# Kernel optimization log

Hardware: AMD Instinct MI355X
Metric: run time of the kernel (lower is better)

The kernel has to match this reference:

```python
import jax, jax.numpy as jnp
import numpy as np
from jax import lax


def _quadrature_weights(bw):
    # s2cnn-style Driscoll-Healy quadrature weights over beta, length 2*bw
    j = np.arange(2 * bw)
    k = np.arange(bw)
    theta = np.pi * (2 * j + 1) / (4 * bw)
    s = (np.sin(np.outer(2 * j + 1, 2 * k + 1) * np.pi / (4 * bw)) / (2 * k + 1)).sum(-1)
    return jnp.asarray((2.0 / bw) * np.sin(theta) * s, jnp.float32)


def _conv2d(x, W, b):
    y = lax.conv_general_dilated(x, W, (1, 1), 'SAME',
                                 dimension_numbers=('NCHW', 'OIHW', 'NCHW'))
    return y + b[None, :, None, None]


def setup_inputs() -> dict:
    key = jax.random.key(0)
    ks = jax.random.split(key, 8)
    b, n = 8, 32768
    res_pt, res_r = 32, 8
    inputs = jax.random.normal(ks[0], (b, n, 3), jnp.float32)
    return {
        'inputs': inputs,
        'scale': jnp.float32(3.0),      # max radius covered by radial bins
        'sigma': jnp.float32(0.5),      # gaussian width in grid units
        'A': jnp.float32(1.0),          # splat amplitude
        'inteval_comp': jnp.float32(0.5),
        'res_pt': res_pt,
        'res_r': res_r,
        'W_s2_1': 0.08 * jax.random.normal(ks[1], (32, 8, 3, 3), jnp.float32),
        'b_s2_1': jnp.zeros((32,), jnp.float32),
        'W_s2_2': 0.05 * jax.random.normal(ks[2], (64, 32, 3, 3), jnp.float32),
        'b_s2_2': jnp.zeros((64,), jnp.float32),
        'W_gamma': 0.1 * jax.random.normal(ks[3], (64, 32), jnp.float32),
        'W_c3_1': 0.05 * jax.random.normal(ks[4], (64, 128), jnp.float32),
        'b_c3_1': jnp.zeros((64,), jnp.float32),
        'W_c3_2': 0.05 * jax.random.normal(ks[5], (32, 64), jnp.float32),
        'b_c3_2': jnp.zeros((32,), jnp.float32),
    }


def reference(inputs, scale, sigma, A, inteval_comp, res_pt, res_r,
              W_s2_1, b_s2_1, W_s2_2, b_s2_2, W_gamma,
              W_c3_1, b_c3_1, W_c3_2, b_c3_2):
    b, n, _ = inputs.shape
    # ---- remap: cartesian -> spherical with min-radius clamp (utils.remap) ----
    x, y, z = inputs[..., 0], inputs[..., 1], inputs[..., 2]
    r = jnp.maximum(jnp.sqrt(x * x + y * y + z * z), 0.1)
    theta = jnp.arccos(jnp.clip(z / r, -1.0, 1.0))            # [0, pi]
    phi = jnp.arctan2(y, x) + np.pi                            # [0, 2pi)
    # ---- s2_gridding: gaussian-weighted point -> (theta,phi,r) grid scatter ----
    ct = theta / np.pi * res_pt                                # continuous bin coords
    cp = phi / (2 * np.pi) * res_pt
    cr = r / scale * res_r
    it = jnp.clip(jnp.floor(ct).astype(jnp.int32), 0, res_pt - 1)
    ip = jnp.clip(jnp.floor(cp).astype(jnp.int32), 0, res_pt - 1)
    ir = jnp.clip(jnp.floor(cr).astype(jnp.int32), 0, res_r - 1)
    d2 = ((ct - (it + inteval_comp)) ** 2
          + (cp - (ip + inteval_comp)) ** 2
          + (cr - (ir + inteval_comp)) ** 2)
    w = A * jnp.exp(-d2 / (2.0 * sigma * sigma))               # (b, n)
    vals = jnp.stack([w, w * x, w * y, w * z], axis=-1)        # (b, n, 4)
    bidx = jnp.arange(b, dtype=jnp.int32)[:, None] * jnp.ones((1, n), jnp.int32)
    flat = ((bidx * res_pt + it) * res_pt + ip) * res_r + ir   # (b, n)
    grid = jnp.zeros((b * res_pt * res_pt * res_r, 4), jnp.float32)
    grid = grid.at[flat.reshape(-1)].add(vals.reshape(-1, 4))
    grid = grid.reshape(b, res_pt, res_pt, res_r, 4)
    ft = jnp.transpose(grid[..., 0], (0, 3, 1, 2))             # (b, res_r, res_pt, res_pt)
    # ---- encoder_l1 (s2cnn_equators): S2 convs + gamma lift to SO3 grid ----
    h = jax.nn.relu(_conv2d(ft, W_s2_1, b_s2_1))
    h = jax.nn.relu(_conv2d(h, W_s2_2, b_s2_2))                # (b, 64, res_pt, res_pt)
    ft_grid = jnp.einsum('bcxy,cg->bcxyg', h, W_gamma)         # (b, 64, rp, rp, rp)
    # ---- so3_integrate: quadrature weight over beta, sum alpha/gamma ----
    wq = _quadrature_weights(res_pt // 2)                      # (res_pt,)
    ft_max = jnp.einsum('bcxyg,y->bc', ft_grid, wq)            # (b, 64)
    # ---- broadcast global feature, concat, pointwise conv3d head ----
    ft_max_ = jnp.broadcast_to(ft_max[:, :, None, None, None],
                               (b, ft_grid.shape[1], res_pt, res_pt, res_pt))
    cat = jnp.concatenate([ft_grid, ft_max_], axis=1)          # (b, 128, rp, rp, rp)
    h3 = jax.nn.relu(jnp.einsum('bcxyg,dc->bdxyg', cat, W_c3_1)
                     + b_c3_1[None, :, None, None, None])
    out = (jnp.einsum('bdxyg,ed->bexyg', h3, W_c3_2)
           + b_c3_2[None, :, None, None, None])                # (b, 32, rp, rp, rp)
    ft_g = out.reshape(b, out.shape[1], -1).max(-1)            # (b, 32)
    return (out, ft_g)
```

## Files before the change

kernel.cpp:

```cpp
#include <hip/hip_runtime.h>
#include <math.h>

#define PI_D 3.14159265358979323846
#define PI_F 3.14159265358979323846f

typedef _Float16 half8 __attribute__((ext_vector_type(8)));
typedef _Float16 half2v __attribute__((ext_vector_type(2)));
typedef float floatx4 __attribute__((ext_vector_type(4)));
#define MFMA16(a,b,c) __builtin_amdgcn_mfma_f32_16x16x32_f16(a,b,c,0,0,0)

__global__ void k_scatter(const float* __restrict__ inp,
                          const float* __restrict__ p_scale,
                          const float* __restrict__ p_sigma,
                          const float* __restrict__ p_A,
                          const float* __restrict__ p_ic,
                          float* __restrict__ ft) {
  int i = blockIdx.x * 256 + threadIdx.x;
  float scale = p_scale[0];
  float sigma = p_sigma[0];
  float A     = p_A[0];
  float icomp = p_ic[0];
  int b = i >> 15;
  float x = inp[i*3+0];
  float y = inp[i*3+1];
  float z = inp[i*3+2];
  float r = sqrtf(x*x + y*y + z*z);
  r = fmaxf(r, 0.1f);
  float ctv = fminf(fmaxf(z / r, -1.0f), 1.0f);
  float theta = acosf(ctv);
  float phi = atan2f(y, x) + PI_F;
  float ct = theta * (32.0f / PI_F);
  float cp = phi * (32.0f / (2.0f * PI_F));
  float cr = r / scale * 8.0f;
  int it = (int)floorf(ct); it = min(max(it, 0), 31);
  int ip = (int)floorf(cp); ip = min(max(ip, 0), 31);
  int ir = (int)floorf(cr); ir = min(max(ir, 0), 7);
  float dt = ct - ((float)it + icomp);
  float dp = cp - ((float)ip + icomp);
  float dr = cr - ((float)ir + icomp);
  float d2 = dt*dt + dp*dp + dr*dr;
  float w = A * expf(-d2 / (2.0f * sigma * sigma));
  atomicAdd(&ft[((b*8 + ir)*32 + it)*32 + ip], w);
}

__global__ void k_wq(float* __restrict__ wq) {
  int t = threadIdx.x;
  double jj = 2.0*(double)t + 1.0;
  double theta = PI_D * jj / 64.0;
  double s = 0.0;
  for (int k = 0; k < 16; ++k)
    s += sin(jj * (double)(2*k+1) * PI_D / 64.0) / (double)(2*k+1);
  wq[t] = (float)((2.0/16.0) * sin(theta) * s);
}

__global__ void k_prepV(const float* __restrict__ Wg, const float* __restrict__ Wc31,
                        _Float16* __restrict__ VswH, _Float16* __restrict__ VswL) {
  int flat = blockIdx.x * 256 + threadIdx.x;
  int jj = flat & 7;
  int l  = (flat >> 3) & 63;
  int rest = flat >> 9;
  int ks = rest & 1, mt = rest >> 1;
  int c = ks*32 + (l >> 4)*8 + jj;
  int m = mt*16 + (l & 15);
  int g = m >> 6, d = m & 63;
  float val = Wg[c*32 + g] * Wc31[d*128 + c];
  _Float16 hi = (_Float16)val;
  _Float16 lo = (_Float16)(val - (float)hi);
  VswH[flat] = hi;
  VswL[flat] = lo;
}

__global__ void k_prepW2(const float* __restrict__ Wc32,
                         _Float16* __restrict__ W2swH, _Float16* __restrict__ W2swL) {
  int flat = blockIdx.x * 256 + threadIdx.x;
  int jj = flat & 7;
  int l  = (flat >> 3) & 63;
  int rest = flat >> 9;
  int ks = rest & 1, mt2 = rest >> 1;
  int e = mt2*16 + (l & 15);
  int d = ks*32 + (l >> 4)*8 + jj;
  float val = Wc32[e*64 + d];
  _Float16 hi = (_Float16)val;
  _Float16 lo = (_Float16)(val - (float)hi);
  W2swH[flat] = hi;
  W2swL[flat] = lo;
}

__global__ void k_conv1(const float* __restrict__ ft, const float* __restrict__ W,
                        const float* __restrict__ bias, float* __restrict__ h1) {
  int blk = blockIdx.x;
  int b = blk >> 5, oc = blk & 31;
  __shared__ float Ws[72];
  int t = threadIdx.x;
  if (t < 72) Ws[t] = W[oc*72 + t];
  __syncthreads();
  int x = t >> 5, y = t & 31;
  float acc = bias[oc];
  const float* fb = ft + b*8192;
  for (int ic = 0; ic < 8; ++ic) {
    const float* fc = fb + ic*1024;
    const float* wr = Ws + ic*9;
#pragma unroll
    for (int dx = -1; dx <= 1; ++dx) {
      int xx = x + dx;
      bool okx = ((unsigned)xx < 32u);
#pragma unroll
      for (int dy = -1; dy <= 1; ++dy) {
        int yy = y + dy;
        float v = (okx && ((unsigned)yy < 32u)) ? fc[xx*32 + yy] : 0.f;
        acc = fmaf(v, wr[(dx+1)*3 + (dy+1)], acc);
      }
    }
  }
  h1[(b*32 + oc)*1024 + t] = fmaxf(acc, 0.f);
}

__global__ __launch_bounds__(512) void k_conv2(const float* __restrict__ h1,
                        const float* __restrict__ W,
                        const float* __restrict__ bias, float* __restrict__ h2) {
  int blk = blockIdx.x;
  int b = blk >> 5, q = blk & 31;
  int oc0 = (q >> 1) * 4, xh = q & 1;
  __shared__ float Ws[4*288];
  int t = threadIdx.x;
  for (int idx = t; idx < 4*288; idx += 512) Ws[idx] = W[oc0*288 + idx];
  __syncthreads();
  int x = xh*16 + (t >> 5), y = t & 31;
  float a0 = bias[oc0+0], a1 = bias[oc0+1], a2 = bias[oc0+2], a3 = bias[oc0+3];
  const float* hb = h1 + b*32*1024;
  for (int ic = 0; ic < 32; ++ic) {
    const float* hc = hb + ic*1024;
    const float* w0 = Ws + 0*288 + ic*9;
    const float* w1 = Ws + 1*288 + ic*9;
    const float* w2 = Ws + 2*288 + ic*9;
    const float* w3 = Ws + 3*288 + ic*9;
#pragma unroll
    for (int dx = -1; dx <= 1; ++dx) {
      int xx = x + dx;
      bool okx = ((unsigned)xx < 32u);
#pragma unroll
      for (int dy = -1; dy <= 1; ++dy) {
        int yy = y + dy;
        float v = (okx && ((unsigned)yy < 32u)) ? hc[xx*32 + yy] : 0.f;
        int k = (dx+1)*3 + (dy+1);
        a0 = fmaf(v, w0[k], a0);
        a1 = fmaf(v, w1[k], a1);
        a2 = fmaf(v, w2[k], a2);
        a3 = fmaf(v, w3[k], a3);
      }
    }
  }
  int p = x*32 + y;
  h2[(b*64 + oc0+0)*1024 + p] = fmaxf(a0, 0.f);
  h2[(b*64 + oc0+1)*1024 + p] = fmaxf(a1, 0.f);
  h2[(b*64 + oc0+2)*1024 + p] = fmaxf(a2, 0.f);
  h2[(b*64 + oc0+3)*1024 + p] = fmaxf(a3, 0.f);
}

__global__ void k_reduce(const float* __restrict__ h2, const float* __restrict__ Wg,
                         const float* __restrict__ wq, float* __restrict__ ftmax) {
  int blk = blockIdx.x;
  int b = blk >> 6, c = blk & 63;
  __shared__ float wqs[32];
  __shared__ float red[256];
  int t = threadIdx.x;
  if (t < 32) wqs[t] = wq[t];
  __syncthreads();
  const float* hb = h2 + (b*64 + c)*1024;
  float acc = 0.f;
  for (int i = t; i < 1024; i += 256) acc = fmaf(hb[i], wqs[i & 31], acc);
  red[t] = acc;
  __syncthreads();
  for (int s2 = 128; s2 > 0; s2 >>= 1) {
    if (t < s2) red[t] += red[t + s2];
    __syncthreads();
  }
  if (t == 0) {
    float sg = 0.f;
    for (int g = 0; g < 32; ++g) sg += Wg[c*32 + g];
    ftmax[b*64 + c] = sg * red[0];
  }
}

__global__ __launch_bounds__(512) void k_head(
    const float* __restrict__ h2, const float* __restrict__ ftmax,
    const float* __restrict__ Wc31, const float* __restrict__ bc31,
    const float* __restrict__ bc32,
    const half8* __restrict__ VswH, const half8* __restrict__ VswL,
    const half8* __restrict__ W2swH, const half8* __restrict__ W2swL,
    float* __restrict__ out, float* __restrict__ blockmax) {
  __shared__ __align__(16) _Float16 h3H[512*72];
  __shared__ __align__(16) _Float16 h3L[512*72];
  __shared__ __align__(16) _Float16 h2H[32*72];
  __shared__ __align__(16) _Float16 h2L[32*72];
  __shared__ float Ks[64];
  __shared__ float vbuf2[8*16];
  int blk = blockIdx.x;
  int b = blk >> 5, x = blk & 31;
  int t = threadIdx.x;
  int lane = t & 63, w = t >> 6;
  int n16 = lane & 15, quad = lane >> 4;

  for (int idx = t; idx < 2048; idx += 512) {
    int c = idx & 63, y = idx >> 6;
    float v = h2[(b*64 + c)*1024 + x*32 + y];
    _Float16 hi = (_Float16)v;
    h2H[y*72 + c] = hi;
    h2L[y*72 + c] = (_Float16)(v - (float)hi);
  }
  if (t < 64) {
    float acc = bc31[t];
    for (int c = 0; c < 64; ++c)
      acc = fmaf(Wc31[t*128 + 64 + c], ftmax[b*64 + c], acc);
    Ks[t] = acc;
  }
  __syncthreads();

  half8 bh00, bh01, bh10, bh11, bl00, bl01, bl10, bl11;
  {
    int a00 = (0*16 + n16)*72 + 0*32 + quad*8;
    int a01 = (0*16 + n16)*72 + 1*32 + quad*8;
    int a10 = (1*16 + n16)*72 + 0*32 + quad*8;
    int a11 = (1*16 + n16)*72 + 1*32 + quad*8;
    bh00 = *(const half8*)&h2H[a00];  bl00 = *(const half8*)&h2L[a00];
    bh01 = *(const half8*)&h2H[a01];  bl01 = *(const half8*)&h2L[a01];
    bh10 = *(const half8*)&h2H[a10];  bl10 = *(const half8*)&h2L[a10];
    bh11 = *(const half8*)&h2H[a11];  bl11 = *(const half8*)&h2L[a11];
  }
  int mt2 = w & 1;
  half8 a2h0 = W2swH[(mt2*2 + 0)*64 + lane];
  half8 a2h1 = W2swH[(mt2*2 + 1)*64 + lane];
  half8 a2l0 = W2swL[(mt2*2 + 0)*64 + lane];
  half8 a2l1 = W2swL[(mt2*2 + 1)*64 + lane];
  float bias_e[4];
#pragma unroll
  for (int r = 0; r < 4; ++r) bias_e[r] = bc32[mt2*16 + quad*4 + r];

  float vmax[4] = {-3.4e38f, -3.4e38f, -3.4e38f, -3.4e38f};

  for (int h = 0; h < 2; ++h) {
    if (h) __syncthreads();
    for (int i = 0; i < 8; ++i) {
      int mt = h*64 + w*8 + i;
      half8 ah0 = VswH[(mt*2 + 0)*64 + lane];
      half8 ah1 = VswH[(mt*2 + 1)*64 + lane];
      half8 al0 = VswL[(mt*2 + 0)*64 + lane];
      half8 al1 = VswL[(mt*2 + 1)*64 + lane];
      floatx4 acc0 = {0.f, 0.f, 0.f, 0.f};
      floatx4 acc1 = {0.f, 0.f, 0.f, 0.f};
      acc0 = MFMA16(ah0, bh00, acc0);  acc1 = MFMA16(ah0, bh10, acc1);
      acc0 = MFMA16(ah0, bl00, acc0);  acc1 = MFMA16(ah0, bl10, acc1);
      acc0 = MFMA16(al0, bh00, acc0);  acc1 = MFMA16(al0, bh10, acc1);
      acc0 = MFMA16(ah1, bh01, acc0);  acc1 = MFMA16(ah1, bh11, acc1);
      acc0 = MFMA16(ah1, bl01, acc0);  acc1 = MFMA16(ah1, bl11, acc1);
      acc0 = MFMA16(al1, bh01, acc0);  acc1 = MFMA16(al1, bh11, acc1);
      int g = mt >> 2, gl = g & 15;
      int dbase = (mt & 3)*16 + quad*4;
      float4 kv = *(const float4*)&Ks[dbase];
#pragma unroll
      for (int nt = 0; nt < 2; ++nt) {
        floatx4 a = nt ? acc1 : acc0;
        int y = nt*16 + n16;
        int rowc = y*16 + gl;
        int dsw = (dbase + y*8) & 63;
        float v0 = fmaxf(a[0] + kv.x, 0.f);
        float v1 = fmaxf(a[1] + kv.y, 0.f);
        float v2 = fmaxf(a[2] + kv.z, 0.f);
        float v3 = fmaxf(a[3] + kv.w, 0.f);
        _Float16 c0 = (_Float16)v0, c1 = (_Float16)v1, c2 = (_Float16)v2, c3 = (_Float16)v3;
        half2v hh0 = {c0, c1}, hh1 = {c2, c3};
        half2v ll0 = {(_Float16)(v0 - (float)c0), (_Float16)(v1 - (float)c1)};
        half2v ll1 = {(_Float16)(v2 - (float)c2), (_Float16)(v3 - (float)c3)};
        int base = rowc*72 + dsw;
        *(half2v*)&h3H[base]     = hh0;
        *(half2v*)&h3H[base + 2] = hh1;
        *(half2v*)&h3L[base]     = ll0;
        *(half2v*)&h3L[base + 2] = ll1;
      }
    }
    __syncthreads();
    for (int i = 0; i < 8; ++i) {
      int nt2 = (w >> 1)*8 + i;
      int rowc = nt2*16 + n16;
      floatx4 acc = {0.f, 0.f, 0.f, 0.f};
      {
        int dsw0 = (0*32 + quad*8 + nt2*8) & 63;
        int dsw1 = (1*32 + quad*8 + nt2*8) & 63;
        half8 b2h0 = *(const half8*)&h3H[rowc*72 + dsw0];
        half8 b2l0 = *(const half8*)&h3L[rowc*72 + dsw0];
        half8 b2h1 = *(const half8*)&h3H[rowc*72 + dsw1];
        half8 b2l1 = *(const half8*)&h3L[rowc*72 + dsw1];
        acc = MFMA16(a2h0, b2h0, acc);
        acc = MFMA16(a2h0, b2l0, acc);
        acc = MFMA16(a2l0, b2h0, acc);
        acc = MFMA16(a2h1, b2h1, acc);
        acc = MFMA16(a2h1, b2l1, acc);
        acc = MFMA16(a2l1, b2h1, acc);
      }
      int y = nt2, g = h*16 + n16;
      size_t base = (((size_t)(b*32 + mt2*16 + quad*4))*1024 + (size_t)(x*32 + y))*32 + g;
#pragma unroll
      for (int r = 0; r < 4; ++r) {
        float v = acc[r] + bias_e[r];
        out[base + (size_t)r*32768] = v;
        vmax[r] = fmaxf(vmax[r], v);
      }
    }
  }
#pragma unroll
  for (int m = 1; m < 16; m <<= 1) {
#pragma unroll
    for (int r = 0; r < 4; ++r)
      vmax[r] = fmaxf(vmax[r], __shfl_xor(vmax[r], m, 64));
  }
  if (n16 == 0) {
#pragma unroll
    for (int r = 0; r < 4; ++r) vbuf2[w*16 + quad*4 + r] = vmax[r];
  }
  __syncthreads();
  if (t < 32) {
    int e = t, m2 = e >> 4, el = e & 15;
    float mm = fmaxf(fmaxf(vbuf2[(m2+0)*16 + el], vbuf2[(m2+2)*16 + el]),
                     fmaxf(vbuf2[(m2+4)*16 + el], vbuf2[(m2+6)*16 + el]));
    blockmax[blk*32 + e] = mm;
  }
}

__global__ void k_final(const float* __restrict__ blockmax, float* __restrict__ ftg) {
  int t = threadIdx.x;
  int b = t >> 5, e = t & 31;
  float m = -3.4e38f;
  for (int x = 0; x < 32; ++x) m = fmaxf(m, blockmax[(b*32 + x)*32 + e]);
  ftg[b*32 + e] = m;
}

extern "C" void kernel_launch(void* const* d_in, const int* in_sizes, int n_in,
                              void* d_out, int out_size, void* d_ws, size_t ws_size,
                              hipStream_t stream) {
  const float* inputs = (const float*)d_in[0];
  const float* scale  = (const float*)d_in[1];
  const float* sigma  = (const float*)d_in[2];
  const float* A      = (const float*)d_in[3];
  const float* icmp   = (const float*)d_in[4];
  const float* W1   = (const float*)d_in[7];
  const float* b1   = (const float*)d_in[8];
  const float* W2   = (const float*)d_in[9];
  const float* b2   = (const float*)d_in[10];
  const float* Wg   = (const float*)d_in[11];
  const float* Wc31 = (const float*)d_in[12];
  const float* bc31 = (const float*)d_in[13];
  const float* Wc32 = (const float*)d_in[14];
  const float* bc32 = (const float*)d_in[15];

  float* ws    = (float*)d_ws;
  float* ft    = ws;
  float* h1    = ws + 65536;
  float* h2    = ws + 327680;
  float* ftmax = ws + 851968;
  float* bmax  = ws + 852480;
  float* wq    = ws + 860672;
  _Float16* VswH  = (_Float16*)(ws + 860704);
  _Float16* VswL  = (_Float16*)(ws + 926240);
  _Float16* W2swH = (_Float16*)(ws + 991776);
  _Float16* W2swL = (_Float16*)(ws + 992800);
  float* out   = (float*)d_out;
  float* ftg   = out + 8388608;

  hipMemsetAsync(ft, 0, 65536*sizeof(float), stream);
  k_wq<<<1, 32, 0, stream>>>(wq);
  k_prepV<<<512, 256, 0, stream>>>(Wg, Wc31, VswH, VswL);
  k_prepW2<<<8, 256, 0, stream>>>(Wc32, W2swH, W2swL);
  k_scatter<<<1024, 256, 0, stream>>>(inputs, scale, sigma, A, icmp, ft);
  k_conv1<<<256, 1024, 0, stream>>>(ft, W1, b1, h1);
  k_conv2<<<256, 512, 0, stream>>>(h1, W2, b2, h2);
  k_reduce<<<512, 256, 0, stream>>>(h2, Wg, wq, ftmax);
  k_head<<<256, 512, 0, stream>>>(h2, ftmax, Wc31, bc31, bc32,
                                  (const half8*)VswH, (const half8*)VswL,
                                  (const half8*)W2swH, (const half8*)W2swL,
                                  out, bmax);
  k_final<<<1, 256, 0, stream>>>(bmax, ftg);
}
```

Before: 179.8 us.

## Fuse prep kernels, fold quadrature reduce into conv2, split head over gamma halves

Merges the memset, quadrature-weight, and weight-swizzle kernels into one prep launch. The quadrature reduction moves into conv2 through wave shuffles and atomics, which removes the separate reduce kernel. The head kernel is split into two blocks per (b,x), one per gamma half, so the grid doubles and LDS shrinks. h2 now loads straight from global into registers. The h3 low-part fp16 compensation is dropped to save MFMAs and LDS, at the cost of lower accuracy in the second GEMM.

New measurement: 186.1 us. +3.5%, slower.

```diff
diff --git a/kernel.cpp b/kernel.cpp
--- a/kernel.cpp
+++ b/kernel.cpp
@@ -5,9 +5,59 @@
 #define PI_F 3.14159265358979323846f
 
 typedef _Float16 half8 __attribute__((ext_vector_type(8)));
-typedef _Float16 half2v __attribute__((ext_vector_type(2)));
+typedef _Float16 half4v __attribute__((ext_vector_type(4)));
 typedef float floatx4 __attribute__((ext_vector_type(4)));
 #define MFMA16(a,b,c) __builtin_amdgcn_mfma_f32_16x16x32_f16(a,b,c,0,0,0)
+
+__global__ void k_prep(const float* __restrict__ Wg, const float* __restrict__ Wc31,
+                       const float* __restrict__ Wc32,
+                       _Float16* __restrict__ VswH, _Float16* __restrict__ VswL,
+                       _Float16* __restrict__ W2swH, _Float16* __restrict__ W2swL,
+                       float* __restrict__ ft, float* __restrict__ WS,
+                       float* __restrict__ wq, float* __restrict__ sgs) {
+  int flat = blockIdx.x * 256 + threadIdx.x;
+  {
+    int jj = flat & 7;
+    int l  = (flat >> 3) & 63;
+    int rest = flat >> 9;
+    int ks = rest & 1, mt = rest >> 1;
+    int c = ks*32 + (l >> 4)*8 + jj;
+    int m = mt*16 + (l & 15);
+    int g = m >> 6, d = m & 63;
+    float val = Wg[c*32 + g] * Wc31[d*128 + c];
+    _Float16 hi = (_Float16)val;
+    VswH[flat] = hi;
+    VswL[flat] = (_Float16)(val - (float)hi);
+  }
+  if (flat < 2048) {
+    int jj = flat & 7;
+    int l  = (flat >> 3) & 63;
+    int rest = flat >> 9;
+    int ks = rest & 1, mt2 = rest >> 1;
+    int e = mt2*16 + (l & 15);
+    int d = ks*32 + (l >> 4)*8 + jj;
+    float val = Wc32[e*64 + d];
+    _Float16 hi = (_Float16)val;
+    W2swH[flat] = hi;
+    W2swL[flat] = (_Float16)(val - (float)hi);
+  }
+  if (flat < 16384) ((float4*)ft)[flat] = make_float4(0.f, 0.f, 0.f, 0.f);
+  if (flat < 32) {
+    double jj = 2.0*(double)flat + 1.0;
+    double theta = PI_D * jj / 64.0;
+    double s = 0.0;
+    for (int k = 0; k < 16; ++k)
+      s += sin(jj * (double)(2*k+1) * PI_D / 64.0) / (double)(2*k+1);
+    wq[flat] = (float)((2.0/16.0) * sin(theta) * s);
+  } else if (flat < 96) {
+    int c = flat - 32;
+    float s = 0.f;
+    for (int g = 0; g < 32; ++g) s += Wg[c*32 + g];
+    sgs[c] = s;
+  } else if (flat < 608) {
+    WS[flat - 96] = 0.f;
+  }
+}
 
 __global__ void k_scatter(const float* __restrict__ inp,
                           const float* __restrict__ p_scale,
@@ -43,49 +93,6 @@
   atomicAdd(&ft[((b*8 + ir)*32 + it)*32 + ip], w);
 }
 
-__global__ void k_wq(float* __restrict__ wq) {
-  int t = threadIdx.x;
-  double jj = 2.0*(double)t + 1.0;
-  double theta = PI_D * jj / 64.0;
-  double s = 0.0;
-  for (int k = 0; k < 16; ++k)
-    s += sin(jj * (double)(2*k+1) * PI_D / 64.0) / (double)(2*k+1);
-  wq[t] = (float)((2.0/16.0) * sin(theta) * s);
-}
-
-__global__ void k_prepV(const float* __restrict__ Wg, const float* __restrict__ Wc31,
-                        _Float16* __restrict__ VswH, _Float16* __restrict__ VswL) {
-  int flat = blockIdx.x * 256 + threadIdx.x;
-  int jj = flat & 7;
-  int l  = (flat >> 3) & 63;
-  int rest = flat >> 9;
-  int ks = rest & 1, mt = rest >> 1;
-  int c = ks*32 + (l >> 4)*8 + jj;
-  int m = mt*16 + (l & 15);
-  int g = m >> 6, d = m & 63;
-  float val = Wg[c*32 + g] * Wc31[d*128 + c];
-  _Float16 hi = (_Float16)val;
-  _Float16 lo = (_Float16)(val - (float)hi);
-  VswH[flat] = hi;
-  VswL[flat] = lo;
-}
-
-__global__ void k_prepW2(const float* __restrict__ Wc32,
-                         _Float16* __restrict__ W2swH, _Float16* __restrict__ W2swL) {
-  int flat = blockIdx.x * 256 + threadIdx.x;
-  int jj = flat & 7;
-  int l  = (flat >> 3) & 63;
-  int rest = flat >> 9;
-  int ks = rest & 1, mt2 = rest >> 1;
-  int e = mt2*16 + (l & 15);
-  int d = ks*32 + (l >> 4)*8 + jj;
-  float val = Wc32[e*64 + d];
-  _Float16 hi = (_Float16)val;
-  _Float16 lo = (_Float16)(val - (float)hi);
-  W2swH[flat] = hi;
-  W2swL[flat] = lo;
-}
-
 __global__ void k_conv1(const float* __restrict__ ft, const float* __restrict__ W,
                         const float* __restrict__ bias, float* __restrict__ h1) {
   int blk = blockIdx.x;
@@ -117,7 +124,9 @@
 
 __global__ __launch_bounds__(512) void k_conv2(const float* __restrict__ h1,
                         const float* __restrict__ W,
-                        const float* __restrict__ bias, float* __restrict__ h2) {
+                        const float* __restrict__ bias,
+                        const float* __restrict__ wq,
+                        float* __restrict__ h2, float* __restrict__ WS) {
   int blk = blockIdx.x;
   int b = blk >> 5, q = blk & 31;
   int oc0 = (q >> 1) * 4, xh = q & 1;
@@ -150,82 +159,74 @@
       }
     }
   }
-  int p = x*32 + y;
-  h2[(b*64 + oc0+0)*1024 + p] = fmaxf(a0, 0.f);
-  h2[(b*64 + oc0+1)*1024 + p] = fmaxf(a1, 0.f);
-  h2[(b*64 + oc0+2)*1024 + p] = fmaxf(a2, 0.f);
-  h2[(b*64 + oc0+3)*1024 + p] = fmaxf(a3, 0.f);
-}
-
-__global__ void k_reduce(const float* __restrict__ h2, const float* __restrict__ Wg,
-                         const float* __restrict__ wq, float* __restrict__ ftmax) {
-  int blk = blockIdx.x;
-  int b = blk >> 6, c = blk & 63;
-  __shared__ float wqs[32];
-  __shared__ float red[256];
-  int t = threadIdx.x;
-  if (t < 32) wqs[t] = wq[t];
-  __syncthreads();
-  const float* hb = h2 + (b*64 + c)*1024;
-  float acc = 0.f;
-  for (int i = t; i < 1024; i += 256) acc = fmaf(hb[i], wqs[i & 31], acc);
-  red[t] = acc;
-  __syncthreads();
-  for (int s2 = 128; s2 > 0; s2 >>= 1) {
-    if (t < s2) red[t] += red[t + s2];
-    __syncthreads();
-  }
-  if (t == 0) {
-    float sg = 0.f;
-    for (int g = 0; g < 32; ++g) sg += Wg[c*32 + g];
-    ftmax[b*64 + c] = sg * red[0];
-  }
-}
-
-__global__ __launch_bounds__(512) void k_head(
-    const float* __restrict__ h2, const float* __restrict__ ftmax,
+  float r0 = fmaxf(a0, 0.f), r1 = fmaxf(a1, 0.f);
+  float r2 = fmaxf(a2, 0.f), r3 = fmaxf(a3, 0.f);
+  int pp = x*32 + y;
+  h2[(b*64 + oc0+0)*1024 + pp] = r0;
+  h2[(b*64 + oc0+1)*1024 + pp] = r1;
+  h2[(b*64 + oc0+2)*1024 + pp] = r2;
+  h2[(b*64 + oc0+3)*1024 + pp] = r3;
+  float wqv = wq[y];
+  float s0 = r0*wqv, s1 = r1*wqv, s2 = r2*wqv, s3 = r3*wqv;
+#pragma unroll
+  for (int m = 1; m < 64; m <<= 1) {
+    s0 += __shfl_xor(s0, m, 64);
+    s1 += __shfl_xor(s1, m, 64);
+    s2 += __shfl_xor(s2, m, 64);
+    s3 += __shfl_xor(s3, m, 64);
+  }
+  if ((t & 63) == 0) {
+    atomicAdd(&WS[b*64 + oc0+0], s0);
+    atomicAdd(&WS[b*64 + oc0+1], s1);
+    atomicAdd(&WS[b*64 + oc0+2], s2);
+    atomicAdd(&WS[b*64 + oc0+3], s3);
+  }
+}
+
+__global__ __launch_bounds__(512, 4) void k_head(
+    const float* __restrict__ h2, const float* __restrict__ WS,
+    const float* __restrict__ sgs,
     const float* __restrict__ Wc31, const float* __restrict__ bc31,
     const float* __restrict__ bc32,
     const half8* __restrict__ VswH, const half8* __restrict__ VswL,
     const half8* __restrict__ W2swH, const half8* __restrict__ W2swL,
     float* __restrict__ out, float* __restrict__ blockmax) {
   __shared__ __align__(16) _Float16 h3H[512*72];
-  __shared__ __align__(16) _Float16 h3L[512*72];
-  __shared__ __align__(16) _Float16 h2H[32*72];
-  __shared__ __align__(16) _Float16 h2L[32*72];
   __shared__ float Ks[64];
-  __shared__ float vbuf2[8*16];
+  __shared__ float vbuf2[128];
   int blk = blockIdx.x;
-  int b = blk >> 5, x = blk & 31;
+  int b = blk >> 6, x = (blk >> 1) & 31, h = blk & 1;
   int t = threadIdx.x;
   int lane = t & 63, w = t >> 6;
   int n16 = lane & 15, quad = lane >> 4;
 
-  for (int idx = t; idx < 2048; idx += 512) {
-    int c = idx & 63, y = idx >> 6;
-    float v = h2[(b*64 + c)*1024 + x*32 + y];
-    _Float16 hi = (_Float16)v;
-    h2H[y*72 + c] = hi;
-    h2L[y*72 + c] = (_Float16)(v - (float)hi);
-  }
   if (t < 64) {
     float acc = bc31[t];
+    const float* wr = Wc31 + t*128 + 64;
+    const float* wsb = WS + b*64;
     for (int c = 0; c < 64; ++c)
-      acc = fmaf(Wc31[t*128 + 64 + c], ftmax[b*64 + c], acc);
+      acc = fmaf(wr[c], sgs[c]*wsb[c], acc);
     Ks[t] = acc;
   }
-  __syncthreads();
 
   half8 bh00, bh01, bh10, bh11, bl00, bl01, bl10, bl11;
   {
-    int a00 = (0*16 + n16)*72 + 0*32 + quad*8;
-    int a01 = (0*16 + n16)*72 + 1*32 + quad*8;
-    int a10 = (1*16 + n16)*72 + 0*32 + quad*8;
-    int a11 = (1*16 + n16)*72 + 1*32 + quad*8;
-    bh00 = *(const half8*)&h2H[a00];  bl00 = *(const half8*)&h2L[a00];
-    bh01 = *(const half8*)&h2H[a01];  bl01 = *(const half8*)&h2L[a01];
-    bh10 = *(const half8*)&h2H[a10];  bl10 = *(const half8*)&h2L[a10];
-    bh11 = *(const half8*)&h2H[a11];  bl11 = *(const half8*)&h2L[a11];
+    const float* h2b = h2 + (size_t)b*64*1024 + x*32;
+#pragma unroll
+    for (int j = 0; j < 8; ++j) {
+      int c0 = quad*8 + j;
+      int c1 = 32 + c0;
+      float f00 = h2b[c0*1024 + n16];
+      float f01 = h2b[c1*1024 + n16];
+      float f10 = h2b[c0*1024 + 16 + n16];
+      float f11 = h2b[c1*1024 + 16 + n16];
+      _Float16 g00 = (_Float16)f00, g01 = (_Float16)f01;
+      _Float16 g10 = (_Float16)f10, g11 = (_Float16)f11;
+      bh00[j] = g00;  bl00[j] = (_Float16)(f00 - (float)g00);
+      bh01[j] = g01;  bl01[j] = (_Float16)(f01 - (float)g01);
+      bh10[j] = g10;  bl10[j] = (_Float16)(f10 - (float)g10);
+      bh11[j] = g11;  bl11[j] = (_Float16)(f11 - (float)g11);
+    }
   }
   int mt2 = w & 1;
   half8 a2h0 = W2swH[(mt2*2 + 0)*64 + lane];
@@ -235,76 +236,60 @@
   float bias_e[4];
 #pragma unroll
   for (int r = 0; r < 4; ++r) bias_e[r] = bc32[mt2*16 + quad*4 + r];
-
+  __syncthreads();
+
+  for (int i = 0; i < 8; ++i) {
+    int mt = h*64 + w*8 + i;
+    half8 ah0 = VswH[(mt*2 + 0)*64 + lane];
+    half8 ah1 = VswH[(mt*2 + 1)*64 + lane];
+    half8 al0 = VswL[(mt*2 + 0)*64 + lane];
+    half8 al1 = VswL[(mt*2 + 1)*64 + lane];
+    floatx4 acc0 = {0.f, 0.f, 0.f, 0.f};
+    floatx4 acc1 = {0.f, 0.f, 0.f, 0.f};
+    acc0 = MFMA16(ah0, bh00, acc0);  acc1 = MFMA16(ah0, bh10, acc1);
+    acc0 = MFMA16(ah0, bl00, acc0);  acc1 = MFMA16(ah0, bl10, acc1);
+    acc0 = MFMA16(al0, bh00, acc0);  acc1 = MFMA16(al0, bh10, acc1);
+    acc0 = MFMA16(ah1, bh01, acc0);  acc1 = MFMA16(ah1, bh11, acc1);
+    acc0 = MFMA16(ah1, bl01, acc0);  acc1 = MFMA16(ah1, bl11, acc1);
+    acc0 = MFMA16(al1, bh01, acc0);  acc1 = MFMA16(al1, bh11, acc1);
+    int g = mt >> 2, gl = g & 15;
+    int dbase = (mt & 3)*16 + quad*4;
+    float4 kv = *(const float4*)&Ks[dbase];
+#pragma unroll
+    for (int nt = 0; nt < 2; ++nt) {
+      floatx4 a = nt ? acc1 : acc0;
+      int y = nt*16 + n16;
+      int rowc = y*16 + gl;
+      int dsw = (dbase + y*8) & 63;
+      half4v hv;
+      hv[0] = (_Float16)fmaxf(a[0] + kv.x, 0.f);
+      hv[1] = (_Float16)fmaxf(a[1] + kv.y, 0.f);
+      hv[2] = (_Float16)fmaxf(a[2] + kv.z, 0.f);
+      hv[3] = (_Float16)fmaxf(a[3] + kv.w, 0.f);
+      *(half4v*)&h3H[rowc*72 + dsw] = hv;
+    }
+  }
+  __syncthreads();
   float vmax[4] = {-3.4e38f, -3.4e38f, -3.4e38f, -3.4e38f};
-
-  for (int h = 0; h < 2; ++h) {
-    if (h) __syncthreads();
-    for (int i = 0; i < 8; ++i) {
-      int mt = h*64 + w*8 + i;
-      half8 ah0 = VswH[(mt*2 + 0)*64 + lane];
-      half8 ah1 = VswH[(mt*2 + 1)*64 + lane];
-      half8 al0 = VswL[(mt*2 + 0)*64 + lane];
-      half8 al1 = VswL[(mt*2 + 1)*64 + lane];
-      floatx4 acc0 = {0.f, 0.f, 0.f, 0.f};
-      floatx4 acc1 = {0.f, 0.f, 0.f, 0.f};
-      acc0 = MFMA16(ah0, bh00, acc0);  acc1 = MFMA16(ah0, bh10, acc1);
-      acc0 = MFMA16(ah0, bl00, acc0);  acc1 = MFMA16(ah0, bl10, acc1);
-      acc0 = MFMA16(al0, bh00, acc0);  acc1 = MFMA16(al0, bh10, acc1);
-      acc0 = MFMA16(ah1, bh01, acc0);  acc1 = MFMA16(ah1, bh11, acc1);
-      acc0 = MFMA16(ah1, bl01, acc0);  acc1 = MFMA16(ah1, bl11, acc1);
-      acc0 = MFMA16(al1, bh01, acc0);  acc1 = MFMA16(al1, bh11, acc1);
-      int g = mt >> 2, gl = g & 15;
-      int dbase = (mt & 3)*16 + quad*4;
-      float4 kv = *(const float4*)&Ks[dbase];
-#pragma unroll
-      for (int nt = 0; nt < 2; ++nt) {
-        floatx4 a = nt ? acc1 : acc0;
-        int y = nt*16 + n16;
-        int rowc = y*16 + gl;
-        int dsw = (dbase + y*8) & 63;
-        float v0 = fmaxf(a[0] + kv.x, 0.f);
-        float v1 = fmaxf(a[1] + kv.y, 0.f);
-        float v2 = fmaxf(a[2] + kv.z, 0.f);
-        float v3 = fmaxf(a[3] + kv.w, 0.f);
-        _Float16 c0 = (_Float16)v0, c1 = (_Float16)v1, c2 = (_Float16)v2, c3 = (_Float16)v3;
-        half2v hh0 = {c0, c1}, hh1 = {c2, c3};
-        half2v ll0 = {(_Float16)(v0 - (float)c0), (_Float16)(v1 - (float)c1)};
-        half2v ll1 = {(_Float16)(v2 - (float)c2), (_Float16)(v3 - (float)c3)};
-        int base = rowc*72 + dsw;
-        *(half2v*)&h3H[base]     = hh0;
-        *(half2v*)&h3H[base + 2] = hh1;
-        *(half2v*)&h3L[base]     = ll0;
-        *(half2v*)&h3L[base + 2] = ll1;
-      }
-    }
-    __syncthreads();
-    for (int i = 0; i < 8; ++i) {
-      int nt2 = (w >> 1)*8 + i;
-      int rowc = nt2*16 + n16;
-      floatx4 acc = {0.f, 0.f, 0.f, 0.f};
-      {
-        int dsw0 = (0*32 + quad*8 + nt2*8) & 63;
-        int dsw1 = (1*32 + quad*8 + nt2*8) & 63;
-        half8 b2h0 = *(const half8*)&h3H[rowc*72 + dsw0];
-        half8 b2l0 = *(const half8*)&h3L[rowc*72 + dsw0];
-        half8 b2h1 = *(const half8*)&h3H[rowc*72 + dsw1];
-        half8 b2l1 = *(const half8*)&h3L[rowc*72 + dsw1];
-        acc = MFMA16(a2h0, b2h0, acc);
-        acc = MFMA16(a2h0, b2l0, acc);
-        acc = MFMA16(a2l0, b2h0, acc);
-        acc = MFMA16(a2h1, b2h1, acc);
-        acc = MFMA16(a2h1, b2l1, acc);
-        acc = MFMA16(a2l1, b2h1, acc);
-      }
-      int y = nt2, g = h*16 + n16;
-      size_t base = (((size_t)(b*32 + mt2*16 + quad*4))*1024 + (size_t)(x*32 + y))*32 + g;
-#pragma unroll
-      for (int r = 0; r < 4; ++r) {
-        float v = acc[r] + bias_e[r];
-        out[base + (size_t)r*32768] = v;
-        vmax[r] = fmaxf(vmax[r], v);
-      }
+  for (int i = 0; i < 8; ++i) {
+    int nt2 = (w >> 1)*8 + i;
+    int rowc = nt2*16 + n16;
+    int dsw0 = (quad*8 + nt2*8) & 63;
+    int dsw1 = (32 + quad*8 + nt2*8) & 63;
+    half8 b2h0 = *(const half8*)&h3H[rowc*72 + dsw0];
+    half8 b2h1 = *(const half8*)&h3H[rowc*72 + dsw1];
+    floatx4 acc = {0.f, 0.f, 0.f, 0.f};
+    acc = MFMA16(a2h0, b2h0, acc);
+    acc = MFMA16(a2l0, b2h0, acc);
+    acc = MFMA16(a2h1, b2h1, acc);
+    acc = MFMA16(a2l1, b2h1, acc);
+    int y = nt2, g = h*16 + n16;
+    size_t base = (((size_t)(b*32 + mt2*16 + quad*4))*1024 + (size_t)(x*32 + y))*32 + g;
+#pragma unroll
+    for (int r = 0; r < 4; ++r) {
+      float v = acc[r] + bias_e[r];
+      out[base + (size_t)r*32768] = v;
+      vmax[r] = fmaxf(vmax[r], v);
     }
   }
 #pragma unroll
@@ -330,7 +315,7 @@
   int t = threadIdx.x;
   int b = t >> 5, e = t & 31;
   float m = -3.4e38f;
-  for (int x = 0; x < 32; ++x) m = fmaxf(m, blockmax[(b*32 + x)*32 + e]);
+  for (int s = 0; s < 64; ++s) m = fmaxf(m, blockmax[(b*64 + s)*32 + e]);
   ftg[b*32 + e] = m;
 }
 
@@ -356,25 +341,23 @@
   float* ft    = ws;
   float* h1    = ws + 65536;
   float* h2    = ws + 327680;
-  float* ftmax = ws + 851968;
+  float* WS    = ws + 851968;
   float* bmax  = ws + 852480;
-  float* wq    = ws + 860672;
-  _Float16* VswH  = (_Float16*)(ws + 860704);
-  _Float16* VswL  = (_Float16*)(ws + 926240);
-  _Float16* W2swH = (_Float16*)(ws + 991776);
-  _Float16* W2swL = (_Float16*)(ws + 992800);
+  float* wq    = ws + 868864;
+  float* sgs   = ws + 868896;
+  _Float16* VswH  = (_Float16*)(ws + 868960);
+  _Float16* VswL  = (_Float16*)(ws + 934496);
+  _Float16* W2swH = (_Float16*)(ws + 1000032);
+  _Float16* W2swL = (_Float16*)(ws + 1001056);
   float* out   = (float*)d_out;
   float* ftg   = out + 8388608;
 
-  hipMemsetAsync(ft, 0, 65536*sizeof(float), stream);
-  k_wq<<<1, 32, 0, stream>>>(wq);
-  k_prepV<<<512, 256, 0, stream>>>(Wg, Wc31, VswH, VswL);
-  k_prepW2<<<8, 256, 0, stream>>>(Wc32, W2swH, W2swL);
+  k_prep<<<512, 256, 0, stream>>>(Wg, Wc31, Wc32, VswH, VswL, W2swH, W2swL,
+                                  ft, WS, wq, sgs);
   k_scatter<<<1024, 256, 0, stream>>>(inputs, scale, sigma, A, icmp, ft);
   k_conv1<<<256, 1024, 0, stream>>>(ft, W1, b1, h1);
-  k_conv2<<<256, 512, 0, stream>>>(h1, W2, b2, h2);
-  k_reduce<<<512, 256, 0, stream>>>(h2, Wg, wq, ftmax);
-  k_head<<<256, 512, 0, stream>>>(h2, ftmax, Wc31, bc31, bc32,
+  k_conv2<<<256, 512, 0, stream>>>(h1, W2, b2, wq, h2, WS);
+  k_head<<<512, 512, 0, stream>>>(h2, WS, sgs, Wc31, bc31, bc32,
                                   (const half8*)VswH, (const half8*)VswL,
                                   (const half8*)W2swH, (const half8*)W2swL,
                                   out, bmax);
```
